# Kernel tuning notes

Hardware: AMD Instinct MI355X
Metric: run time of the kernel (lower is better)

## Reference

```python
import jax, jax.numpy as jnp
import numpy as np

NHEADS = 16


def setup_inputs() -> dict:
    key = jax.random.key(0)
    k1, k2, k3 = jax.random.split(key, 3)
    b, t, d = 4, 1024, 1024
    x = jax.random.normal(k1, (b, t, d), dtype=jnp.float32)
    mask = jnp.ones((b, t), dtype=bool)
    # torch Linear weights: [out_features, in_features], custom uniform init std ~ init_std/sqrt(d/3)
    std = 1.0 / np.sqrt(d)
    W_in = jax.random.uniform(k2, (3 * d, d), dtype=jnp.float32, minval=-std, maxval=std)
    W_out = jax.random.uniform(k3, (d, d), dtype=jnp.float32, minval=-std, maxval=std)
    return {"x": x, "mask": mask, "W_in": W_in, "W_out": W_out}


def reference(x, mask, W_in, W_out):
    b, t, d = x.shape
    h = NHEADS
    hd = d // h
    # QKV projection (no bias)
    qkv = x @ W_in.T                       # [b, t, 3d]
    q, k, v = jnp.split(qkv, 3, axis=-1)   # each [b, t, d]

    def to_heads(y):
        return y.reshape(b, t, h, hd).transpose(0, 2, 1, 3)  # [b, h, t, hd]

    q, k, v = to_heads(q), to_heads(k), to_heads(v)

    # padding mask [b, tq, tk] = valid_q & valid_k, then causal tril
    pad = mask[:, :, None] & mask[:, None, :]
    causal = jnp.tril(jnp.ones((t, t), dtype=bool))
    keep = pad & causal[None]
    bias = jnp.where(keep, 0.0, -jnp.inf).astype(x.dtype)[:, None]  # [b, 1, t, t]

    scale = 1.0 / np.sqrt(hd)
    scores = jnp.einsum('bhqd,bhkd->bhqk', q, k) * scale + bias  # [b, h, t, t]
    probs = jax.nn.softmax(scores, axis=-1)
    out = jnp.einsum('bhqk,bhkd->bhqd', probs, v)                # [b, h, t, hd]
    out = out.transpose(0, 2, 1, 3).reshape(b, t, d)
    out = out @ W_out.T
    # TensorMask.apply_mask: zero out padded positions
    out = out * mask[:, :, None].astype(out.dtype)
    return out
```

## Files before the change

### kernel.cpp

```cpp
#include <hip/hip_runtime.h>

typedef __attribute__((ext_vector_type(8))) short bf16x8;
typedef __attribute__((ext_vector_type(4))) float f32x4;
typedef __attribute__((ext_vector_type(16))) float f32x16;

#define GAS __attribute__((address_space(1)))
#define LAS __attribute__((address_space(3)))

static __device__ __forceinline__ unsigned short f2bf(float f) {
  unsigned int u = __builtin_bit_cast(unsigned int, f);
  u += 0x7fffu + ((u >> 16) & 1u);
  return (unsigned short)(u >> 16);
}

static __device__ __forceinline__ unsigned int pk2(float a, float b) {
  unsigned int r;
  asm("v_cvt_pk_bf16_f32 %0, %1, %2" : "=v"(r) : "v"(a), "v"(b));
  return r;
}

__global__ __launch_bounds__(256) void cvt_all(const float* __restrict__ x,
                                               const float* __restrict__ wi,
                                               const float* __restrict__ wo,
                                               unsigned short* __restrict__ xb,
                                               unsigned short* __restrict__ wib,
                                               unsigned short* __restrict__ wob) {
  const int i = blockIdx.x * 256 + threadIdx.x;
  const float* in;
  unsigned short* out;
  int j;
  if (i < 1048576)      { in = x;  out = xb;  j = i; }
  else if (i < 1835008) { in = wi; out = wib; j = i - 1048576; }
  else                  { in = wo; out = wob; j = i - 1835008; }
  float4 v = reinterpret_cast<const float4*>(in)[j];
  ushort4 o;
  o.x = f2bf(v.x); o.y = f2bf(v.y); o.z = f2bf(v.z); o.w = f2bf(v.w);
  reinterpret_cast<ushort4*>(out)[j] = o;
}

template <int EPI, int GXSH, int BN>
static __device__ __forceinline__ void gemm_body(const unsigned short* __restrict__ A,
                                                 const unsigned short* __restrict__ Bt,
                                                 int K,
                                                 unsigned short* __restrict__ qkv,
                                                 float* __restrict__ outf,
                                                 int bid, int nblk,
                                                 unsigned short* __restrict__ AsB,
                                                 unsigned short* __restrict__ BsB) {
  constexpr int NB = BN / 32;
  constexpr int BPASS = BN / 64;
  const int chunk = nblk >> 3;
  const int sw = (bid & 7) * chunk + (bid >> 3);
  const int bx = sw & ((1 << GXSH) - 1), by = sw >> GXSH;
  const int m0 = by * 128, n0 = bx * BN;

  const int tid = threadIdx.x;
  const int lane = tid & 63;
  const int w = tid >> 6, wr = w >> 1, wc = w & 1;
  const int l15 = lane & 15, g = lane >> 4;
  const int ks = g * 8;

  f32x4 acc[4][NB] = {};

  auto stage = [&](int buf, int k0) {
#pragma unroll
    for (int is = 0; is < 2; ++is) {
      const int e = is * 2048 + tid * 8;
      const int row = e >> 5, kk = e & 31;
      const unsigned short* gA = A + (size_t)(m0 + row) * K + (k0 + kk);
      unsigned short* lA = AsB + buf * 4096 + ((tid & ~63) * 8 + is * 2048);
      __builtin_amdgcn_global_load_lds((const GAS void*)gA, (LAS void*)lA, 16, 0, 0);
    }
#pragma unroll
    for (int is = 0; is < BPASS; ++is) {
      const int e = is * 2048 + tid * 8;
      const int row = e >> 5, kk = e & 31;
      const unsigned short* gB = Bt + (size_t)(n0 + row) * K + (k0 + kk);
      unsigned short* lB = BsB + buf * (BN * 32) + ((tid & ~63) * 8 + is * 2048);
      __builtin_amdgcn_global_load_lds((const GAS void*)gB, (LAS void*)lB, 16, 0, 0);
    }
  };

  const int nt = K >> 5;
  stage(0, 0);
  stage(1, 1 << 5);
  stage(2, 2 << 5);
  int buf = 0;
  for (int t = 0; t < nt; ++t) {
    if constexpr (BPASS == 2) {
      if (t + 2 < nt)      asm volatile("s_waitcnt vmcnt(8)" ::: "memory");
      else if (t + 1 < nt) asm volatile("s_waitcnt vmcnt(4)" ::: "memory");
      else                 asm volatile("s_waitcnt vmcnt(0)" ::: "memory");
    } else {
      if (t + 2 < nt)      asm volatile("s_waitcnt vmcnt(6)" ::: "memory");
      else if (t + 1 < nt) asm volatile("s_waitcnt vmcnt(3)" ::: "memory");
      else                 asm volatile("s_waitcnt vmcnt(0)" ::: "memory");
    }
    __builtin_amdgcn_s_barrier();

    bf16x8 a[4], b[NB];
#pragma unroll
    for (int mi = 0; mi < 4; ++mi)
      a[mi] = *reinterpret_cast<const bf16x8*>(
          &AsB[buf * 4096 + (wr * 64 + mi * 16 + l15) * 32 + ks]);
#pragma unroll
    for (int ni = 0; ni < NB; ++ni)
      b[ni] = *reinterpret_cast<const bf16x8*>(
          &BsB[buf * (BN * 32) + (wc * (BN / 2) + ni * 16 + l15) * 32 + ks]);
#pragma unroll
    for (int mi = 0; mi < 4; ++mi)
#pragma unroll
      for (int ni = 0; ni < NB; ++ni)
        acc[mi][ni] = __builtin_amdgcn_mfma_f32_16x16x32_bf16(a[mi], b[ni], acc[mi][ni], 0, 0, 0);

    __builtin_amdgcn_s_barrier();
    if (t + 3 < nt) stage(buf, (t + 3) << 5);
    if (++buf == 3) buf = 0;
  }

#pragma unroll
  for (int mi = 0; mi < 4; ++mi) {
#pragma unroll
    for (int ni = 0; ni < NB; ++ni) {
      const int col = n0 + wc * (BN / 2) + ni * 16 + l15;
#pragma unroll
      for (int r = 0; r < 4; ++r) {
        const int row = m0 + wr * 64 + mi * 16 + g * 4 + r;
        const float v = acc[mi][ni][r];
        if (EPI == 0) {
          const int which = col >> 10, d = col & 1023;
          const int hh = d >> 6, hd = d & 63;
          const int bb = row >> 10, tt = row & 1023;
          const float sc = (which == 0) ? 0.18033688011112042f : 1.0f;
          qkv[(size_t)which * 4194304 +
              (((size_t)bb * 16 + hh) * 1024 + (size_t)tt) * 64 + hd] = f2bf(v * sc);
        } else if (EPI == 2) {
          const int hh = row >> 6, hd = row & 63;
          const int bb = col >> 10, tt = col & 1023;
          const int tp = (tt & ~12) | ((tt & 8) >> 1) | ((tt & 4) << 1);
          qkv[(((size_t)bb * 16 + hh) * 64 + hd) * 1024 + tp] = f2bf(v);
        } else {
          outf[(size_t)row * 1024 + col] = v;
        }
      }
    }
  }
}

__global__ __launch_bounds__(256, 3) void gemm_qkv(const unsigned short* __restrict__ xb,
                                                   const unsigned short* __restrict__ wib,
                                                   unsigned short* __restrict__ qh,
                                                   unsigned short* __restrict__ vh) {
  __shared__ __align__(16) unsigned short As[3][4096];
  __shared__ __align__(16) unsigned short Bs[3][4096];
  const int bid = blockIdx.x;
  if (bid < 512) {
    gemm_body<0, 4, 128>(xb, wib, 1024, qh, nullptr, bid, 512, &As[0][0], &Bs[0][0]);
  } else {
    gemm_body<2, 5, 128>(wib + 2048 * 1024, xb, 1024, vh, nullptr, bid - 512, 256,
                         &As[0][0], &Bs[0][0]);
  }
}

__global__ __launch_bounds__(256, 2) void gemm_out(const unsigned short* __restrict__ A,
                                                   const unsigned short* __restrict__ Bt,
                                                   float* __restrict__ outf) {
  __shared__ __align__(16) unsigned short As[3][4096];
  __shared__ __align__(16) unsigned short Bs[3][2048];
  gemm_body<1, 4, 64>(A, Bt, 1024, nullptr, outf, blockIdx.x, gridDim.x,
                      &As[0][0], &Bs[0][0]);
}

__global__ __launch_bounds__(256, 2) void attn_kernel(const unsigned short* __restrict__ qh,
                                                      const unsigned short* __restrict__ kh,
                                                      const unsigned short* __restrict__ vt,
                                                      unsigned short* __restrict__ ao) {
  __shared__ __align__(16) unsigned short Ks[3][2][2048];
  __shared__ __align__(16) unsigned short Vs[3][2][2048];

  const int bid = blockIdx.x;
  int qb, bh;
  if (bid < 256) { qb = 7 - (bid >> 6); bh = bid & 63; }
  else           { const int j = bid - 256; qb = j >> 6; bh = j & 63; }

  const int tid = threadIdx.x, lane = tid & 63, w = tid >> 6;
  const int l31 = lane & 31, hk = lane >> 5;
  const int qt = qb * 4 + w;
  const int qrow = qt * 32 + l31;

  const unsigned short* Q = qh + (size_t)bh * 65536;
  const unsigned short* Kb = kh + (size_t)bh * 65536;
  const unsigned short* Vt = vt + (size_t)bh * 65536;

  bf16x8 qf[4];
#pragma unroll
  for (int kc = 0; kc < 4; ++kc)
    qf[kc] = *reinterpret_cast<const bf16x8*>(&Q[(size_t)qrow * 64 + kc * 16 + hk * 8]);

  f32x16 o0 = {}, o1 = {};
  f32x16 p0 = {}, p1 = {};
  float lrun = 0.f;

  auto stage64 = [&](int buf, int kv0) {
#pragma unroll
    for (int s = 0; s < 2; ++s) {
      {
        const int r = tid >> 3, cs = (tid & 7) ^ (r & 7);
        const unsigned short* g = Kb + (size_t)(kv0 + s * 32 + r) * 64 + cs * 8;
        unsigned short* l = Ks[buf][s] + (tid & ~63) * 8;
        __builtin_amdgcn_global_load_lds((const GAS void*)g, (LAS void*)l, 16, 0, 0);
      }
      {
        const int b = tid >> 3, F = (tid & 7) ^ (b & 7);
        const unsigned short* g = Vt + (size_t)(2 * b + (F >> 2)) * 1024 +
                                  (kv0 + s * 32) + (F & 3) * 8;
        unsigned short* l = Vs[buf][s] + (tid & ~63) * 8;
        __builtin_amdgcn_global_load_lds((const GAS void*)g, (LAS void*)l, 16, 0, 0);
      }
    }
  };

  auto SM = [&](f32x16& st, unsigned int (&pw)[8]) -> float {
    float psp[8];
#pragma unroll
    for (int j = 0; j < 8; ++j) {
      const float a = exp2f(st[2 * j]);
      const float b = exp2f(st[2 * j + 1]);
      pw[j] = pk2(a, b);
      psp[j] = a + b;
    }
    return ((psp[0] + psp[1]) + (psp[2] + psp[3])) +
           ((psp[4] + psp[5]) + (psp[6] + psp[7]));
  };

  auto TILE1 = [&](int buf) {
    f32x16 st = {};
    __builtin_amdgcn_s_setprio(1);
#pragma unroll
    for (int kc = 0; kc < 4; ++kc) {
      const int cc = kc * 2 + hk;
      const bf16x8 kf = *reinterpret_cast<const bf16x8*>(
          &Ks[buf][0][l31 * 64 + ((cc ^ (l31 & 7)) * 8)]);
      st = __builtin_amdgcn_mfma_f32_32x32x16_bf16(kf, qf[kc], st, 0, 0, 0);
    }
    __builtin_amdgcn_s_setprio(0);
#pragma unroll
    for (int r = 0; r < 16; ++r) {
      const int klocal = (r & 3) + 8 * (r >> 2) + 4 * hk;
      st[r] = (klocal <= l31) ? st[r] : -3e38f;
    }
    unsigned int pw[8];
    lrun += SM(st, pw);
#pragma unroll
    for (int m = 0; m < 2; ++m) {
      union { unsigned int u[4]; bf16x8 v; } pb;
#pragma unroll
      for (int c = 0; c < 4; ++c) pb.u[c] = pw[4 * m + c];
      const int c = 2 * m + hk;
      const int b0 = l31 >> 1;
      const int a0 = b0 * 64 + (((((l31 & 1) << 2) | c) ^ (b0 & 7)) * 8);
      const int b1 = (32 + l31) >> 1;
      const int a1 = b1 * 64 + (((((l31 & 1) << 2) | c) ^ (b1 & 7)) * 8);
      const bf16x8 vf0 = *reinterpret_cast<const bf16x8*>(&Vs[buf][0][a0]);
      const bf16x8 vf1 = *reinterpret_cast<const bf16x8*>(&Vs[buf][0][a1]);
      __builtin_amdgcn_s_setprio(1);
      o0 = __builtin_amdgcn_mfma_f32_32x32x16_bf16(vf0, pb.v, o0, 0, 0, 0);
      o1 = __builtin_amdgcn_mfma_f32_32x32x16_bf16(vf1, pb.v, o1, 0, 0, 0);
      __builtin_amdgcn_s_setprio(0);
    }
  };

  auto TILE2 = [&](int buf, bool diag1) {
    f32x16 st0 = {}, st1 = {};
    __builtin_amdgcn_s_setprio(1);
#pragma unroll
    for (int kc = 0; kc < 4; ++kc) {
      const int cc = kc * 2 + hk;
      const int ka = l31 * 64 + ((cc ^ (l31 & 7)) * 8);
      const bf16x8 kf0 = *reinterpret_cast<const bf16x8*>(&Ks[buf][0][ka]);
      const bf16x8 kf1 = *reinterpret_cast<const bf16x8*>(&Ks[buf][1][ka]);
      st0 = __builtin_amdgcn_mfma_f32_32x32x16_bf16(kf0, qf[kc], st0, 0, 0, 0);
      st1 = __builtin_amdgcn_mfma_f32_32x32x16_bf16(kf1, qf[kc], st1, 0, 0, 0);
    }
    __builtin_amdgcn_s_setprio(0);
    if (diag1) {
#pragma unroll
      for (int r = 0; r < 16; ++r) {
        const int klocal = (r & 3) + 8 * (r >> 2) + 4 * hk;
        st1[r] = (klocal <= l31) ? st1[r] : -3e38f;
      }
    }
    unsigned int pw0[8], pw1[8];
    const float s0 = SM(st0, pw0);
    const float s1 = SM(st1, pw1);
    lrun += s0 + s1;
#pragma unroll
    for (int m = 0; m < 2; ++m) {
      union { unsigned int u[4]; bf16x8 v; } pb0, pb1;
#pragma unroll
      for (int c = 0; c < 4; ++c) { pb0.u[c] = pw0[4 * m + c]; pb1.u[c] = pw1[4 * m + c]; }
      const int c = 2 * m + hk;
      const int b0 = l31 >> 1;
      const int a0 = b0 * 64 + (((((l31 & 1) << 2) | c) ^ (b0 & 7)) * 8);
      const int b1 = (32 + l31) >> 1;
      const int a1 = b1 * 64 + (((((l31 & 1) << 2) | c) ^ (b1 & 7)) * 8);
      const bf16x8 vf00 = *reinterpret_cast<const bf16x8*>(&Vs[buf][0][a0]);
      const bf16x8 vf01 = *reinterpret_cast<const bf16x8*>(&Vs[buf][0][a1]);
      const bf16x8 vf10 = *reinterpret_cast<const bf16x8*>(&Vs[buf][1][a0]);
      const bf16x8 vf11 = *reinterpret_cast<const bf16x8*>(&Vs[buf][1][a1]);
      __builtin_amdgcn_s_setprio(1);
      o0 = __builtin_amdgcn_mfma_f32_32x32x16_bf16(vf00, pb0.v, o0, 0, 0, 0);
      p0 = __builtin_amdgcn_mfma_f32_32x32x16_bf16(vf10, pb1.v, p0, 0, 0, 0);
      o1 = __builtin_amdgcn_mfma_f32_32x32x16_bf16(vf01, pb0.v, o1, 0, 0, 0);
      p1 = __builtin_amdgcn_mfma_f32_32x32x16_bf16(vf11, pb1.v, p1, 0, 0, 0);
      __builtin_amdgcn_s_setprio(0);
    }
  };

  const int nch = (qb * 4 + 4) >> 1;
  const int myt = qt + 1;
  stage64(0, 0);
  if (nch > 1) stage64(1, 64);
  for (int c = 0; c < nch; ++c) {
    if (c + 1 < nch) asm volatile("s_waitcnt vmcnt(4)" ::: "memory");
    else             asm volatile("s_waitcnt vmcnt(0)" ::: "memory");
    __builtin_amdgcn_s_barrier();
    if (c + 2 < nch) stage64((c + 2) % 3, (c + 2) << 6);
    const int t0 = 2 * c;
    if (t0 < myt) {
      if (t0 + 1 < myt) TILE2(c % 3, t0 + 1 == qt);
      else              TILE1(c % 3);
    }
  }

  o0 += p0;
  o1 += p1;

  const float ltot = lrun + __shfl_xor(lrun, 32);
  const float inv = 1.f / ltot;
  const int b = bh >> 4, h = bh & 15;
  const size_t rowbase = ((size_t)(b * 1024 + qrow)) * 1024 + h * 64;
#pragma unroll
  for (int rb = 0; rb < 2; ++rb)
#pragma unroll
    for (int dp = 0; dp < 4; ++dp) {
      ushort4 s;
      const f32x16& o = rb ? o1 : o0;
      s.x = f2bf(o[4 * dp + 0] * inv);
      s.y = f2bf(o[4 * dp + 1] * inv);
      s.z = f2bf(o[4 * dp + 2] * inv);
      s.w = f2bf(o[4 * dp + 3] * inv);
      *reinterpret_cast<ushort4*>(&ao[rowbase + rb * 32 + 8 * dp + 4 * hk]) = s;
    }
}

extern "C" void kernel_launch(void* const* d_in, const int* in_sizes, int n_in,
                              void* d_out, int out_size, void* d_ws, size_t ws_size,
                              hipStream_t stream) {
  const float* x = (const float*)d_in[0];
  const float* W_in = (const float*)d_in[2];
  const float* W_out = (const float*)d_in[3];
  float* out = (float*)d_out;

  unsigned short* ws = (unsigned short*)d_ws;
  unsigned short* xb = ws;
  unsigned short* wib = xb + 4194304;
  unsigned short* wob = wib + 3145728;
  unsigned short* qh = wob + 1048576;
  unsigned short* kh = qh + 4194304;
  unsigned short* vh = kh + 4194304;
  unsigned short* ao = vh + 4194304;

  cvt_all<<<8192, 256, 0, stream>>>(x, W_in, W_out, xb, wib, wob);

  gemm_qkv<<<768, 256, 0, stream>>>(xb, wib, qh, vh);

  attn_kernel<<<512, 256, 0, stream>>>(qh, kh, vh, ao);

  gemm_out<<<512, 256, 0, stream>>>(ao, wob, out);
}
```

Before: 88.37 us.

## Interleave attention query tiles across warps and fold W_out conversion into attention

The attention kernel now gives each warp query tile qb+8*w instead of four consecutive tiles. This balances causal work across blocks but makes every block stream nearly the full K/V range, while its warps finish unevenly. The W_out fp32-to-bf16 conversion moves out of the conversion kernel into 64 extra blocks appended to the attention launch, so it overlaps attention. The remaining conversion kernel now handles 8 elements per thread with 16-byte stores.

```diff
diff --git a/kernel.cpp b/kernel.cpp
--- a/kernel.cpp
+++ b/kernel.cpp
@@ -21,21 +21,20 @@
 
 __global__ __launch_bounds__(256) void cvt_all(const float* __restrict__ x,
                                                const float* __restrict__ wi,
-                                               const float* __restrict__ wo,
                                                unsigned short* __restrict__ xb,
-                                               unsigned short* __restrict__ wib,
-                                               unsigned short* __restrict__ wob) {
+                                               unsigned short* __restrict__ wib) {
   const int i = blockIdx.x * 256 + threadIdx.x;
   const float* in;
   unsigned short* out;
   int j;
-  if (i < 1048576)      { in = x;  out = xb;  j = i; }
-  else if (i < 1835008) { in = wi; out = wib; j = i - 1048576; }
-  else                  { in = wo; out = wob; j = i - 1835008; }
-  float4 v = reinterpret_cast<const float4*>(in)[j];
-  ushort4 o;
-  o.x = f2bf(v.x); o.y = f2bf(v.y); o.z = f2bf(v.z); o.w = f2bf(v.w);
-  reinterpret_cast<ushort4*>(out)[j] = o;
+  if (i < 524288) { in = x;  out = xb;  j = i; }
+  else            { in = wi; out = wib; j = i - 524288; }
+  const float4 v0 = reinterpret_cast<const float4*>(in)[2 * j];
+  const float4 v1 = reinterpret_cast<const float4*>(in)[2 * j + 1];
+  union { ushort4 h[2]; bf16x8 v; } o;
+  o.h[0].x = f2bf(v0.x); o.h[0].y = f2bf(v0.y); o.h[0].z = f2bf(v0.z); o.h[0].w = f2bf(v0.w);
+  o.h[1].x = f2bf(v1.x); o.h[1].y = f2bf(v1.y); o.h[1].z = f2bf(v1.z); o.h[1].w = f2bf(v1.w);
+  reinterpret_cast<bf16x8*>(out)[j] = o.v;
 }
 
 template <int EPI, int GXSH, int BN>
@@ -174,18 +173,35 @@
 __global__ __launch_bounds__(256, 2) void attn_kernel(const unsigned short* __restrict__ qh,
                                                       const unsigned short* __restrict__ kh,
                                                       const unsigned short* __restrict__ vt,
-                                                      unsigned short* __restrict__ ao) {
+                                                      unsigned short* __restrict__ ao,
+                                                      const float* __restrict__ wo,
+                                                      unsigned short* __restrict__ wob) {
   __shared__ __align__(16) unsigned short Ks[3][2][2048];
   __shared__ __align__(16) unsigned short Vs[3][2][2048];
 
   const int bid = blockIdx.x;
+  if (bid >= 512) {
+    const int base = (bid - 512) * 256 + threadIdx.x;
+#pragma unroll
+    for (int it = 0; it < 8; ++it) {
+      const int u = base + it * 16384;
+      const float4 v0 = reinterpret_cast<const float4*>(wo)[2 * u];
+      const float4 v1 = reinterpret_cast<const float4*>(wo)[2 * u + 1];
+      union { ushort4 h[2]; bf16x8 v; } o;
+      o.h[0].x = f2bf(v0.x); o.h[0].y = f2bf(v0.y); o.h[0].z = f2bf(v0.z); o.h[0].w = f2bf(v0.w);
+      o.h[1].x = f2bf(v1.x); o.h[1].y = f2bf(v1.y); o.h[1].z = f2bf(v1.z); o.h[1].w = f2bf(v1.w);
+      reinterpret_cast<bf16x8*>(wob)[u] = o.v;
+    }
+    return;
+  }
+
   int qb, bh;
   if (bid < 256) { qb = 7 - (bid >> 6); bh = bid & 63; }
   else           { const int j = bid - 256; qb = j >> 6; bh = j & 63; }
 
   const int tid = threadIdx.x, lane = tid & 63, w = tid >> 6;
   const int l31 = lane & 31, hk = lane >> 5;
-  const int qt = qb * 4 + w;
+  const int qt = qb + 8 * w;
   const int qrow = qt * 32 + l31;
 
   const unsigned short* Q = qh + (size_t)bh * 65536;
@@ -317,10 +333,10 @@
     }
   };
 
-  const int nch = (qb * 4 + 4) >> 1;
+  const int nch = (qb + 26) >> 1;
   const int myt = qt + 1;
   stage64(0, 0);
-  if (nch > 1) stage64(1, 64);
+  stage64(1, 64);
   for (int c = 0; c < nch; ++c) {
     if (c + 1 < nch) asm volatile("s_waitcnt vmcnt(4)" ::: "memory");
     else             asm volatile("s_waitcnt vmcnt(0)" ::: "memory");
@@ -371,11 +387,11 @@
   unsigned short* vh = kh + 4194304;
   unsigned short* ao = vh + 4194304;
 
-  cvt_all<<<8192, 256, 0, stream>>>(x, W_in, W_out, xb, wib, wob);
+  cvt_all<<<3584, 256, 0, stream>>>(x, W_in, xb, wib);
 
   gemm_qkv<<<768, 256, 0, stream>>>(xb, wib, qh, vh);
 
-  attn_kernel<<<512, 256, 0, stream>>>(qh, kh, vh, ao);
+  attn_kernel<<<576, 256, 0, stream>>>(qh, kh, vh, ao, W_out, wob);
 
   gemm_out<<<512, 256, 0, stream>>>(ao, wob, out);
 }
```

New measurement: 89.43 us. About the same (+1.2%).
